# Performance work log

Measured on AMD Instinct MI355X. Metric: run time of the kernel, lower is better.

The kernel has to match this reference:

```python
import jax, jax.numpy as jnp
import numpy as np

DIM = 128          # dim (forced by LayerNorm(dim) on last-dim-128 reshape)
NP = 24            # num_patch
N = NP * NP        # 576 tokens
HEADS = 128        # num_heads (forced by einsum contraction, d' must be 1)
HEAD_D = 2         # head_dim
INNER = HEADS * HEAD_D  # 256 (forced by SRA Conv2d(256, ...))
B = 2
SCALE = HEAD_D ** -0.5
EPS = 1e-5


def setup_inputs() -> dict:
    key = jax.random.key(0)
    ks = jax.random.split(key, 12)
    f = jax.random.normal
    return {
        'x': f(ks[0], (B, N, DIM), jnp.float32),
        'bn_gamma': 1.0 + 0.1 * f(ks[1], (DIM,), jnp.float32),
        'bn_beta': 0.1 * f(ks[2], (DIM,), jnp.float32),
        # qkc: Conv2d(128, 768, 1, groups=head_dim=2, bias=False) -> OIHW (768, 64, 1, 1)
        'qkc_w': 0.05 * f(ks[3], (3 * INNER, DIM // HEAD_D, 1, 1), jnp.float32),
        # spe: Conv2d(128, 128, 1, groups=2, bias=False)
        'spe_w': 0.05 * f(ks[4], (DIM, DIM // HEAD_D, 1, 1), jnp.float32),
        # SRA.sr: Conv2d(256, 128, 3, padding=1, groups=128) -> OIHW (128, 2, 3, 3), with bias
        'sr_w': 0.05 * f(ks[5], (DIM, INNER // DIM, 3, 3), jnp.float32),
        'sr_b': 0.01 * f(ks[6], (DIM,), jnp.float32),
        'ln_gamma': 1.0 + 0.1 * f(ks[7], (DIM,), jnp.float32),
        'ln_beta': 0.1 * f(ks[8], (DIM,), jnp.float32),
        # local: Conv2d(128, 128, 3, padding=1, groups=2, bias=False)
        'local_w': 0.05 * f(ks[9], (DIM, DIM // HEAD_D, 3, 3), jnp.float32),
        'bnc1_gamma': 1.0 + 0.1 * f(ks[10], (DIM,), jnp.float32),
        'bnc1_beta': 0.1 * f(ks[11], (DIM,), jnp.float32),
    }


def _conv(x, w, groups, pad):
    return jax.lax.conv_general_dilated(
        x, w, (1, 1), pad,
        dimension_numbers=('NCHW', 'OIHW', 'NCHW'),
        feature_group_count=groups)


def _bn_inf(x, g, b):
    # BatchNorm2d in inference form with running_mean=0, running_var=1
    return x * (g / jnp.sqrt(1.0 + EPS))[None, :, None, None] + b[None, :, None, None]


def reference(x, bn_gamma, bn_beta, qkc_w, spe_w, sr_w, sr_b,
              ln_gamma, ln_beta, local_w, bnc1_gamma, bnc1_beta):
    b = x.shape[0]
    x4 = x.reshape(b, DIM, NP, NP)                       # (b,128,24,24)
    a = jax.nn.gelu(_bn_inf(x4, bn_gamma, bn_beta), approximate=False)

    # qkc grouped 1x1 conv -> (b,768,24,24), raw view to (b,576,768)
    qkv = _conv(a, qkc_w, HEAD_D, 'VALID').reshape(b, N, 3 * INNER)
    v_chunk = qkv[..., 2 * INNER:]                       # only v survives the chained assignment
    # rearrange 'b (h d) n -> b n h d', h=NP : (b,576,256) -> (b,256,24,24)
    v4 = v_chunk.reshape(b, NP, NP, INNER).transpose(0, 3, 1, 2)

    # SRA (sr_ratio = num_heads > 1): grouped 3x3 conv + LayerNorm
    xsr = _conv(v4, sr_w, DIM, ((1, 1), (1, 1))) + sr_b[None, :, None, None]  # (b,128,24,24)
    x_ = xsr.reshape(b, N, DIM)                          # row-major view, matches torch
    mu = x_.mean(-1, keepdims=True)
    var = ((x_ - mu) ** 2).mean(-1, keepdims=True)
    qy = (x_ - mu) / jnp.sqrt(var + EPS) * ln_gamma + ln_beta

    # q = k = v : (b, heads=128, N=576, d'=1)
    q = qy.reshape(b, N, HEADS, 1).transpose(0, 2, 1, 3)

    # spe branch: grouped 1x1 conv + global avg pool -> (b,128,1,1) -> (b,128,1,1) as bh(nw)d
    spe = _conv(a, spe_w, HEAD_D, 'VALID').mean(axis=(2, 3)).reshape(b, HEADS, 1, 1)

    scores = jnp.einsum('bhid,bhjd->bhij', q, q) * SCALE  # (b,128,576,576)
    attn = jax.nn.softmax(scores, axis=-1)

    v_spe = jnp.einsum('bhij,bhjd->bhid', q, spe) * SCALE  # (b,128,576,1)
    v_spe1 = jax.nn.softmax(v_spe, axis=-1)                # size-1 axis -> ones (faithful)
    out = jnp.einsum('bhij,bhjd->bhid', attn, v_spe1)      # (b,128,576,1)
    out = out.transpose(0, 2, 1, 3).reshape(b, N, HEADS)   # 'b h n d -> b n (h d)'

    # local conv branch
    c = jax.nn.gelu(_bn_inf(_conv(x4, local_w, HEAD_D, ((1, 1), (1, 1))),
                            bnc1_gamma, bnc1_beta), approximate=False)
    c = c.reshape(b, N, DIM)                               # raw view, matches torch reshape

    # AdaptiveAvgPool1d(128) on a length-128 last dim is identity
    return out + c
```

## Files before the change

kernel.cpp:

```cpp
#include <hip/hip_runtime.h>
#include <hip/hip_bf16.h>


__global__ __launch_bounds__(576, 1) void fused_conv_gelu(
    const float* __restrict__ x,
    const float* __restrict__ lw,
    const float* __restrict__ gam,
    const float* __restrict__ bet,
    float* __restrict__ out)
{
    const int bi = blockIdx.x;
    const int b  = bi >> 7;
    const int o  = bi & 127;
    const int g  = o >> 6;
    const int p  = threadIdx.x;
    const int h  = p / 24;
    const int w  = p - h * 24;

    const float* __restrict__ xb = x  + (b * 128 + g * 64) * 576;
    const float* __restrict__ wb = lw + o * 576;

    bool val[9];
#pragma unroll
    for (int dh = 0; dh < 3; ++dh)
#pragma unroll
        for (int dw = 0; dw < 3; ++dw) {
            const int hh = h + dh - 1, ww = w + dw - 1;
            val[dh * 3 + dw] = (hh >= 0) && (hh < 24) && (ww >= 0) && (ww < 24);
        }

    float acc = 0.0f;

#pragma unroll
    for (int ic = 0; ic < 2; ++ic) {
        const int i = ic ? 63 : 0;
        const float* __restrict__ xi = xb + i * 576;
        const float* __restrict__ wi = wb + i * 9;
#pragma unroll
        for (int dh = 0; dh < 3; ++dh)
#pragma unroll
            for (int dw = 0; dw < 3; ++dw) {
                const int t  = dh * 3 + dw;
                const int hh = min(max(h + dh - 1, 0), 23);
                const int ww = min(max(w + dw - 1, 0), 23);
                const float xv = xi[hh * 24 + ww];
                acc = fmaf(val[t] ? xv : 0.0f, wi[t], acc);
            }
    }

#pragma unroll 2
    for (int i = 1; i < 63; ++i) {
        const float* __restrict__ xi = xb + i * 576 + p;
        const float* __restrict__ wi = wb + i * 9;
#pragma unroll
        for (int dh = 0; dh < 3; ++dh)
#pragma unroll
            for (int dw = 0; dw < 3; ++dw) {
                const int t  = dh * 3 + dw;
                const float xv = xi[(dh - 1) * 24 + (dw - 1)];
                acc = fmaf(val[t] ? xv : 0.0f, wi[t], acc);
            }
    }

    const float scale = gam[o] * rsqrtf(1.0f + 1e-5f);
    const float shift = bet[o];
    const float y  = fmaf(acc, scale, shift);
    const float gl = 0.5f * y * (1.0f + erff(y * 0.70710678118654752f));
    out[b * 73728 + o * 576 + p] = 1.0f + gl;
}

extern "C" void kernel_launch(void* const* d_in, const int* in_sizes, int n_in,
                              void* d_out, int out_size, void* d_ws, size_t ws_size,
                              hipStream_t stream) {
    const float* x   = (const float*)d_in[0];
    const float* lw  = (const float*)d_in[9];
    const float* gam = (const float*)d_in[10];
    const float* bet = (const float*)d_in[11];
    float* out = (float*)d_out;

    fused_conv_gelu<<<dim3(256), dim3(576), 0, stream>>>(x, lw, gam, bet, out);
}
```

Baseline: 87.29 us.

## Register-block conv over 4 pixels and split input channels across thread groups

Each thread now computes four adjacent output pixels from float4 row loads, reusing each loaded input across several taps. The 64 input channels are split into four groups of 16, one per set of threads, and the partial sums are combined through shared memory. Filter weights are staged in LDS, and boundary masks are folded into the weights. This cuts redundant global loads and shortens the serial channel loop, at the cost of an extra barrier and a shared-memory reduction.

```diff
diff --git a/kernel.cpp b/kernel.cpp
--- a/kernel.cpp
+++ b/kernel.cpp
@@ -1,5 +1,4 @@
 #include <hip/hip_runtime.h>
-#include <hip/hip_bf16.h>
 
 
 __global__ __launch_bounds__(576, 1) void fused_conv_gelu(
@@ -13,60 +12,76 @@
     const int b  = bi >> 7;
     const int o  = bi & 127;
     const int g  = o >> 6;
-    const int p  = threadIdx.x;
-    const int h  = p / 24;
-    const int w  = p - h * 24;
 
-    const float* __restrict__ xb = x  + (b * 128 + g * 64) * 576;
-    const float* __restrict__ wb = lw + o * 576;
+    const int t  = threadIdx.x;
+    const int cs = t / 144;
+    const int q  = t - cs * 144;
+    const int h  = q / 6;
+    const int w0 = (q - h * 6) * 4;
 
-    bool val[9];
-#pragma unroll
-    for (int dh = 0; dh < 3; ++dh)
-#pragma unroll
-        for (int dw = 0; dw < 3; ++dw) {
-            const int hh = h + dh - 1, ww = w + dw - 1;
-            val[dh * 3 + dw] = (hh >= 0) && (hh < 24) && (ww >= 0) && (ww < 24);
-        }
+    __shared__ float wlds[64 * 12];
+    __shared__ float red[4][576];
+    {
+        const int c = t / 9, k = t - c * 9;
+        wlds[c * 12 + k] = lw[o * 576 + t];
+    }
+    __syncthreads();
 
-    float acc = 0.0f;
+    const float m0 = (h > 0)  ? 1.0f : 0.0f;
+    const float m2 = (h < 23) ? 1.0f : 0.0f;
+    const int   hm = (h > 0)  ? h - 1 : 0;
+    const int   hp = (h < 23) ? h + 1 : 23;
+    const bool  lz = (w0 == 0), rz = (w0 == 20);
+    const int   loff = lz ? 0 : -1;
+    const int   roff = rz ? 3 : 4;
 
-#pragma unroll
-    for (int ic = 0; ic < 2; ++ic) {
-        const int i = ic ? 63 : 0;
-        const float* __restrict__ xi = xb + i * 576;
-        const float* __restrict__ wi = wb + i * 9;
-#pragma unroll
-        for (int dh = 0; dh < 3; ++dh)
-#pragma unroll
-            for (int dw = 0; dw < 3; ++dw) {
-                const int t  = dh * 3 + dw;
-                const int hh = min(max(h + dh - 1, 0), 23);
-                const int ww = min(max(w + dw - 1, 0), 23);
-                const float xv = xi[hh * 24 + ww];
-                acc = fmaf(val[t] ? xv : 0.0f, wi[t], acc);
-            }
+    const float* __restrict__ xg = x + (b * 128 + g * 64 + cs * 16) * 576;
+
+    float acc0 = 0.f, acc1 = 0.f, acc2 = 0.f, acc3 = 0.f;
+
+#define CONV_ROW(RP, T0, T1, T2)                                        \
+    {                                                                   \
+        const float4 m4 = *reinterpret_cast<const float4*>(RP);         \
+        float xl = (RP)[loff]; if (lz) xl = 0.f;                        \
+        float xr = (RP)[roff]; if (rz) xr = 0.f;                        \
+        acc0 = fmaf(xl,   T0, acc0);                                    \
+        acc0 = fmaf(m4.x, T1, acc0);                                    \
+        acc0 = fmaf(m4.y, T2, acc0);                                    \
+        acc1 = fmaf(m4.x, T0, acc1);                                    \
+        acc1 = fmaf(m4.y, T1, acc1);                                    \
+        acc1 = fmaf(m4.z, T2, acc1);                                    \
+        acc2 = fmaf(m4.y, T0, acc2);                                    \
+        acc2 = fmaf(m4.z, T1, acc2);                                    \
+        acc2 = fmaf(m4.w, T2, acc2);                                    \
+        acc3 = fmaf(m4.z, T0, acc3);                                    \
+        acc3 = fmaf(m4.w, T1, acc3);                                    \
+        acc3 = fmaf(xr,   T2, acc3);                                    \
     }
 
-#pragma unroll 2
-    for (int i = 1; i < 63; ++i) {
-        const float* __restrict__ xi = xb + i * 576 + p;
-        const float* __restrict__ wi = wb + i * 9;
-#pragma unroll
-        for (int dh = 0; dh < 3; ++dh)
-#pragma unroll
-            for (int dw = 0; dw < 3; ++dw) {
-                const int t  = dh * 3 + dw;
-                const float xv = xi[(dh - 1) * 24 + (dw - 1)];
-                acc = fmaf(val[t] ? xv : 0.0f, wi[t], acc);
-            }
+#pragma unroll 4
+    for (int cc = 0; cc < 16; ++cc) {
+        const float* __restrict__ xc = xg + cc * 576;
+        const int c = cs * 16 + cc;
+        const float4 wA = *reinterpret_cast<const float4*>(&wlds[c * 12]);
+        const float4 wB = *reinterpret_cast<const float4*>(&wlds[c * 12 + 4]);
+        const float  w8 = wlds[c * 12 + 8];
+
+        CONV_ROW(xc + hm * 24 + w0, wA.x * m0, wA.y * m0, wA.z * m0);
+        CONV_ROW(xc + h  * 24 + w0, wA.w,      wB.x,      wB.y);
+        CONV_ROW(xc + hp * 24 + w0, wB.z * m2, wB.w * m2, w8   * m2);
     }
+#undef CONV_ROW
 
+    *reinterpret_cast<float4*>(&red[cs][4 * q]) =
+        make_float4(acc0, acc1, acc2, acc3);
+    __syncthreads();
+
+    const float s = red[0][t] + red[1][t] + red[2][t] + red[3][t];
     const float scale = gam[o] * rsqrtf(1.0f + 1e-5f);
     const float shift = bet[o];
-    const float y  = fmaf(acc, scale, shift);
+    const float y  = fmaf(s, scale, shift);
     const float gl = 0.5f * y * (1.0f + erff(y * 0.70710678118654752f));
-    out[b * 73728 + o * 576 + p] = 1.0f + gl;
+    out[b * 73728 + o * 576 + t] = 1.0f + gl;
 }
 
 extern "C" void kernel_launch(void* const* d_in, const int* in_sizes, int n_in,
```

After: 91.73 us. +5.1%, slower.
